# Optimization experiments

Measured on AMD Instinct MI355X. Metric: run time of the kernel, lower is better.

## Reference

```python
import jax, jax.numpy as jnp
import numpy as np

N_NODES = 100000
N_EDGES = 3200000


def gcn_conv(x, src, dst, W, b, n):
    # x: [N, Fin] -> linear transform then symmetric-normalized scatter-add (PyG GCNConv)
    xw = x @ W  # [N, Fout]
    loop = jnp.arange(n, dtype=src.dtype)
    s = jnp.concatenate([src, loop])  # add self-loops
    d = jnp.concatenate([dst, loop])
    deg = jax.ops.segment_sum(jnp.ones_like(s, dtype=xw.dtype), d, num_segments=n)
    dinv = jnp.where(deg > 0, jax.lax.rsqrt(deg), 0.0)
    norm = dinv[s] * dinv[d]  # [E+N]
    out = jax.ops.segment_sum(xw[s] * norm[:, None], d, num_segments=n)
    return out + b


def setup_inputs() -> dict:
    key = jax.random.key(0)
    ks = jax.random.split(key, 11)
    x = jax.random.normal(ks[0], (N_NODES, 2), dtype=jnp.float32)
    edge_index = jax.random.randint(ks[1], (2, N_EDGES), 0, N_NODES, dtype=jnp.int64)
    W1 = jax.random.normal(ks[2], (2, 32), dtype=jnp.float32) * 0.5
    b1 = jax.random.normal(ks[3], (32,), dtype=jnp.float32) * 0.1
    W2 = jax.random.normal(ks[4], (32, 32), dtype=jnp.float32) * 0.18
    b2 = jax.random.normal(ks[5], (32,), dtype=jnp.float32) * 0.1
    Wf1 = jax.random.normal(ks[6], (32, 32), dtype=jnp.float32) * 0.18
    bf1 = jax.random.normal(ks[7], (32,), dtype=jnp.float32) * 0.1
    Wf2 = jax.random.normal(ks[8], (32, 1), dtype=jnp.float32) * 0.18
    bf2 = jax.random.normal(ks[9], (1,), dtype=jnp.float32) * 0.1
    return {"x": x, "edge_index": edge_index, "W1": W1, "b1": b1, "W2": W2,
            "b2": b2, "Wf1": Wf1, "bf1": bf1, "Wf2": Wf2, "bf2": bf2}


def reference(x, edge_index, W1, b1, W2, b2, Wf1, bf1, Wf2, bf2):
    n = x.shape[0]
    src, dst = edge_index[0], edge_index[1]
    h = jax.nn.relu(gcn_conv(x, src, dst, W1, b1, n))
    h = jax.nn.relu(gcn_conv(h, src, dst, W2, b2, n))
    h = jax.nn.relu(h @ Wf1 + bf1)
    return h @ Wf2 + bf2  # [N, 1]
```

## Files before the change

### kernel.cpp

```cpp
#include <hip/hip_runtime.h>

#define NGRP 512
#define CAP  7424
#define PTHREADS 1024
#define NE   16
#define EPB  (PTHREADS * NE)
#define SRC_BITS 17
#define SRC_MASK 0x1FFFF

static __device__ __forceinline__ unsigned f2bf(float f) {
    unsigned u = __float_as_uint(f);
    return (u + 0x7FFFu + ((u >> 16) & 1u)) >> 16;
}
static __device__ __forceinline__ float bf2f_lo(unsigned u) { return __uint_as_float(u << 16); }
static __device__ __forceinline__ float bf2f_hi(unsigned u) { return __uint_as_float(u & 0xFFFF0000u); }


__global__ __launch_bounds__(PTHREADS) void k_partition(const int* __restrict__ ei, int* gcursor,
                                                        unsigned* __restrict__ pairs,
                                                        int E, int n, int GN) {
    __shared__ int cnt[NGRP];
    __shared__ int cur[NGRP];
    int tid = threadIdx.x;
    if (tid < NGRP) cnt[tid] = 0;
    __syncthreads();
    int base = blockIdx.x * EPB;
    int sreg[NE], dreg[NE];
#pragma unroll
    for (int k = 0; k < NE; ++k) {
        int e = base + tid + k * PTHREADS;
        int d = -1, s = 0;
        if (e < E) {
            s = ei[e];
            d = ei[E + e];
            if ((unsigned)s < (unsigned)n && (unsigned)d < (unsigned)n)
                atomicAdd(&cnt[d / GN], 1);
            else d = -1;
        }
        sreg[k] = s; dreg[k] = d;
    }
    __syncthreads();
    if (tid < NGRP) {
        int c = cnt[tid];
        int rel = c ? atomicAdd(&gcursor[tid], c) : 0;
        cur[tid] = tid * CAP + rel;
    }
    __syncthreads();
#pragma unroll
    for (int k = 0; k < NE; ++k) {
        int d = dreg[k];
        if (d >= 0) {
            int g = d / GN;
            int w = atomicAdd(&cur[g], 1);
            if (w < (g + 1) * CAP)
                pairs[w] = ((unsigned)(d - g * GN) << SRC_BITS) | (unsigned)sreg[k];
        }
    }
}

__global__ __launch_bounds__(512) void k_build(const int* __restrict__ gcursor,
                                               const unsigned* __restrict__ pairs,
                                               const float2* __restrict__ x2,
                                               int* __restrict__ rowStart, int* __restrict__ rowEnd,
                                               int* __restrict__ srclist, float* __restrict__ dinv,
                                               float2* __restrict__ z, int n, int GN) {
    __shared__ unsigned pl[CAP];
    __shared__ int cnt[512];
    __shared__ int cur[512];
    int g = blockIdx.x;
    int t = threadIdx.x;
    int gbeg = g * CAP;
    int m = gcursor[g];
    const int MCAP = CAP - 600;
    if (m > MCAP) m = MCAP;
    cnt[t] = 0;
    if (g == 0 && t == 0) z[n] = make_float2(0.f, 0.f);
    __syncthreads();
    for (int k = t; k < m; k += 512) {
        unsigned v = pairs[gbeg + k];
        pl[k] = v;
        atomicAdd(&cnt[(v >> SRC_BITS) & 511], 1);
    }
    __syncthreads();
    int c = cnt[t];
    int rnd = (c + 3) & ~3;
    __syncthreads();
    cnt[t] = rnd;
    __syncthreads();
    for (int off = 1; off < 512; off <<= 1) {
        int add = (t >= off) ? cnt[t - off] : 0;
        __syncthreads();
        cnt[t] += add;
        __syncthreads();
    }
    int excl = cnt[t] - rnd;
    int node = g * GN + t;
    int st = gbeg + excl;
    if (t < GN && node < n) {
        rowStart[node] = st;
        rowEnd[node] = st + rnd;
        float di = rsqrtf(1.0f + (float)c);
        dinv[node] = di;
        float2 xv = x2[node];
        z[node] = make_float2(xv.x * di, xv.y * di);
        for (int j = c; j < rnd; ++j) srclist[st + j] = n;
    }
    cur[t] = excl;
    __syncthreads();
    for (int k = t; k < m; k += 512) {
        unsigned v = pl[k];
        int dl = (v >> SRC_BITS) & 511;
        int pos = atomicAdd(&cur[dl], 1);
        srclist[gbeg + pos] = (int)(v & SRC_MASK);
    }
}


__global__ __launch_bounds__(256) void k_mid1f(const int* __restrict__ rowStart,
                                               const int* __restrict__ rowEnd,
                                               const int* __restrict__ srclist,
                                               const float2* __restrict__ z,
                                               const float* __restrict__ dinv,
                                               const float* __restrict__ W1,
                                               const float* __restrict__ b1,
                                               const float* __restrict__ W2,
                                               unsigned short* __restrict__ y0,
                                               unsigned short* __restrict__ y1, int n) {
    __shared__ float sW[1024];
    __shared__ float sh[8][33];
    int tid = threadIdx.x;
    for (int k = tid; k < 1024; k += 256) sW[k] = W2[k];
    int ln = tid >> 5, f = tid & 31;
    int i = blockIdx.x * 8 + ln;
    float ax = 0.f, ay = 0.f;
    if (i < n) {
        int e = rowStart[i] + f, end = rowEnd[i];
        for (; e < end; e += 32) {
            float2 v = z[srclist[e]];
            ax += v.x; ay += v.y;
        }
    }
#pragma unroll
    for (int m = 1; m < 32; m <<= 1) {
        ax += __shfl_xor(ax, m, 64);
        ay += __shfl_xor(ay, m, 64);
    }
    float h = 0.f, di = 0.f;
    if (i < n) {
        di = dinv[i];
        float2 zz = z[i];
        ax += zz.x; ay += zz.y;
        h = di * (ax * W1[f] + ay * W1[32 + f]) + b1[f];
        h = h > 0.f ? h : 0.f;
    }
    sh[ln][f] = h;
    __syncthreads();
    if (i < n) {
        float acc = 0.f;
#pragma unroll
        for (int k = 0; k < 32; ++k) acc += sh[ln][k] * sW[k * 32 + f];
        unsigned short* ypl = (f < 16) ? y0 : y1;
        ypl[(size_t)i * 16 + (f & 15)] = (unsigned short)f2bf(acc * di);
    } else if (i == n) {
        unsigned short* ypl = (f < 16) ? y0 : y1;
        ypl[(size_t)n * 16 + (f & 15)] = 0;
    }
}

#define ACC8(v)                                        \
    a0 += bf2f_lo((v).x); a1 += bf2f_hi((v).x);        \
    a2 += bf2f_lo((v).y); a3 += bf2f_hi((v).y);        \
    a4 += bf2f_lo((v).z); a5 += bf2f_hi((v).z);        \
    a6 += bf2f_lo((v).w); a7 += bf2f_hi((v).w);

__global__ __launch_bounds__(256) void k_gather_planes(const int* __restrict__ rowStart,
                                                       const int* __restrict__ rowEnd,
                                                       const int* __restrict__ srclist,
                                                       const uint4* __restrict__ yp0,
                                                       const uint4* __restrict__ yp1,
                                                       const float* __restrict__ dinv,
                                                       const float* __restrict__ b2,
                                                       unsigned short* __restrict__ h2_0,
                                                       unsigned short* __restrict__ h2_1,
                                                       int n, int nb) {
    int blk = blockIdx.x;
    int p = (blk >> 2) & 1;
    int b = (blk >> 3) * 4 + (blk & 3);
    if (b >= nb) return;
    const uint4* yh = p ? yp1 : yp0;
    unsigned short* hp = p ? h2_1 : h2_0;
    int w = b * 64 + (threadIdx.x >> 2);
    if (w >= n) return;
    int slot = (threadIdx.x >> 1) & 1;
    int q = threadIdx.x & 1;
    int beg = rowStart[w];
    int nq = (rowEnd[w] - beg) >> 2;
    const int4* sl4 = (const int4*)(srclist + beg);
    float a0 = 0.f, a1 = 0.f, a2 = 0.f, a3 = 0.f, a4 = 0.f, a5 = 0.f, a6 = 0.f, a7 = 0.f;
    for (int j = slot; j < nq; j += 2) {
        int4 s4 = sl4[j];
        uint4 v0 = yh[(size_t)s4.x * 2 + q];
        uint4 v1 = yh[(size_t)s4.y * 2 + q];
        uint4 v2 = yh[(size_t)s4.z * 2 + q];
        uint4 v3 = yh[(size_t)s4.w * 2 + q];
        ACC8(v0); ACC8(v1); ACC8(v2); ACC8(v3);
    }
    if (slot == 0) {
        uint4 v = yh[(size_t)w * 2 + q];
        ACC8(v);
    }
    a0 += __shfl_xor(a0, 2, 64);
    a1 += __shfl_xor(a1, 2, 64);
    a2 += __shfl_xor(a2, 2, 64);
    a3 += __shfl_xor(a3, 2, 64);
    a4 += __shfl_xor(a4, 2, 64);
    a5 += __shfl_xor(a5, 2, 64);
    a6 += __shfl_xor(a6, 2, 64);
    a7 += __shfl_xor(a7, 2, 64);
    if (slot == 0) {
        float di = dinv[w];
        const float* bb = b2 + p * 16 + q * 8;
        float t0 = di * a0 + bb[0]; t0 = t0 > 0.f ? t0 : 0.f;
        float t1 = di * a1 + bb[1]; t1 = t1 > 0.f ? t1 : 0.f;
        float t2 = di * a2 + bb[2]; t2 = t2 > 0.f ? t2 : 0.f;
        float t3 = di * a3 + bb[3]; t3 = t3 > 0.f ? t3 : 0.f;
        float t4 = di * a4 + bb[4]; t4 = t4 > 0.f ? t4 : 0.f;
        float t5 = di * a5 + bb[5]; t5 = t5 > 0.f ? t5 : 0.f;
        float t6 = di * a6 + bb[6]; t6 = t6 > 0.f ? t6 : 0.f;
        float t7 = di * a7 + bb[7]; t7 = t7 > 0.f ? t7 : 0.f;
        uint4 pk;
        pk.x = f2bf(t0) | (f2bf(t1) << 16);
        pk.y = f2bf(t2) | (f2bf(t3) << 16);
        pk.z = f2bf(t4) | (f2bf(t5) << 16);
        pk.w = f2bf(t6) | (f2bf(t7) << 16);
        *(uint4*)(hp + (size_t)w * 16 + q * 8) = pk;
    }
}

__global__ void k_final(const unsigned short* __restrict__ h2_0,
                        const unsigned short* __restrict__ h2_1,
                        const float* __restrict__ Wf1, const float* __restrict__ bf1,
                        const float* __restrict__ Wf2, const float* __restrict__ bf2,
                        float* __restrict__ out, int n) {
    __shared__ float sW[1024];
    __shared__ float sh[8][33];
    int tid = threadIdx.x;
    for (int k = tid; k < 1024; k += 256) sW[k] = Wf1[k];
    int ln = tid >> 5, f = tid & 31;
    int i = blockIdx.x * 8 + ln;
    float h = 0.f;
    if (i < n) {
        const unsigned short* hp = (f < 16) ? h2_0 : h2_1;
        unsigned short u = hp[(size_t)i * 16 + (f & 15)];
        h = __uint_as_float((unsigned)u << 16);
    }
    sh[ln][f] = h;
    __syncthreads();
    float p = 0.f;
    if (i < n) {
        float a = bf1[f];
#pragma unroll
        for (int k = 0; k < 32; ++k) a += sh[ln][k] * sW[k * 32 + f];
        a = a > 0.f ? a : 0.f;
        p = a * Wf2[f];
    }
#pragma unroll
    for (int m = 16; m >= 1; m >>= 1) p += __shfl_xor(p, m, 64);
    if (f == 0 && i < n) out[i] = p + bf2[0];
}


extern "C" void kernel_launch(void* const* d_in, const int* in_sizes, int n_in,
                              void* d_out, int out_size, void* d_ws, size_t ws_size,
                              hipStream_t stream) {
    const float* x   = (const float*)d_in[0];
    const int*   ei  = (const int*)d_in[1];
    const float* W1  = (const float*)d_in[2];
    const float* b1  = (const float*)d_in[3];
    const float* W2  = (const float*)d_in[4];
    const float* b2  = (const float*)d_in[5];
    const float* Wf1 = (const float*)d_in[6];
    const float* bf1 = (const float*)d_in[7];
    const float* Wf2 = (const float*)d_in[8];
    const float* bf2 = (const float*)d_in[9];
    float* out = (float*)d_out;

    int n = in_sizes[0] / 2;
    int E = in_sizes[1] / 2;
    int GN = (n + NGRP - 1) / NGRP;

    char* wp = (char*)d_ws;
    auto alloc = [&](size_t bytes) {
        char* ptr = wp;
        wp += (bytes + 15) & ~(size_t)15;
        return ptr;
    };
    int*      srclist = (int*)     alloc(sizeof(int) * (size_t)NGRP * CAP);
    unsigned* pairs   = (unsigned*)alloc(sizeof(unsigned) * (size_t)NGRP * CAP);
    int*      rowStart= (int*)     alloc(sizeof(int) * (size_t)n);
    int*      rowEnd  = (int*)     alloc(sizeof(int) * (size_t)n);
    float*    dinv    = (float*)   alloc(sizeof(float) * (size_t)n);
    float2*   z       = (float2*)  alloc(sizeof(float2) * (size_t)(n + 1));
    int*      gcursor = (int*)     alloc(sizeof(int) * NGRP);
    unsigned short* y0  = (unsigned short*)alloc(2 * (size_t)(n + 1) * 16);
    unsigned short* y1  = (unsigned short*)alloc(2 * (size_t)(n + 1) * 16);
    unsigned short* h2_0= (unsigned short*)alloc(2 * (size_t)n * 16);
    unsigned short* h2_1= (unsigned short*)alloc(2 * (size_t)n * 16);

    int nblk = (E + EPB - 1) / EPB;
    int nb = (n + 63) / 64;
    int nsg = (nb + 3) / 4;

    (void)hipMemsetAsync(gcursor, 0, NGRP * sizeof(int), stream);
    k_partition<<<nblk, PTHREADS, 0, stream>>>(ei, gcursor, pairs, E, n, GN);
    k_build<<<NGRP, 512, 0, stream>>>(gcursor, pairs, (const float2*)x, rowStart, rowEnd,
                                      srclist, dinv, z, n, GN);

    k_mid1f<<<(n + 8) / 8, 256, 0, stream>>>(rowStart, rowEnd, srclist, z, dinv,
                                             W1, b1, W2, y0, y1, n);

    k_gather_planes<<<nsg * 8, 256, 0, stream>>>(rowStart, rowEnd, srclist,
                                                 (const uint4*)y0, (const uint4*)y1,
                                                 dinv, b2, h2_0, h2_1, n, nb);

    k_final<<<(n + 7) / 8, 256, 0, stream>>>(h2_0, h2_1, Wf1, bf1, Wf2, bf2, out, n);
}
```

Before: 160.0 us.

## Replicate partition counters and split layer-1 gather into thread-per-node kernel

The partition kernel now keeps four replicas of the per-group shared counters and cursors, indexed by thread lane, to reduce LDS atomic contention. The first-layer aggregation is split out of the fused kernel into its own kernel that assigns one thread per node, reads sources four at a time with int4 loads, and writes a float2 aggregate. A separate kernel then applies W1, ReLU and W2. This avoids leaving most of a 32-lane group idle on rows averaging about 32 edges, at the cost of an extra launch and a round trip of the aggregate through global memory. The int4 loop assumes each row's padded length is a multiple of four and that row starts are 16-byte aligned.

```diff
diff --git a/kernel.cpp b/kernel.cpp
--- a/kernel.cpp
+++ b/kernel.cpp
@@ -5,6 +5,7 @@
 #define PTHREADS 1024
 #define NE   16
 #define EPB  (PTHREADS * NE)
+#define NREP 4
 #define SRC_BITS 17
 #define SRC_MASK 0x1FFFF
 
@@ -19,10 +20,11 @@
 __global__ __launch_bounds__(PTHREADS) void k_partition(const int* __restrict__ ei, int* gcursor,
                                                         unsigned* __restrict__ pairs,
                                                         int E, int n, int GN) {
-    __shared__ int cnt[NGRP];
-    __shared__ int cur[NGRP];
+    __shared__ int cnt[NGRP][NREP];
+    __shared__ int cur[NGRP][NREP];
     int tid = threadIdx.x;
-    if (tid < NGRP) cnt[tid] = 0;
+    int r = tid & (NREP - 1);
+    for (int k = tid; k < NGRP * NREP; k += PTHREADS) ((int*)cnt)[k] = 0;
     __syncthreads();
     int base = blockIdx.x * EPB;
     int sreg[NE], dreg[NE];
@@ -34,16 +36,21 @@
             s = ei[e];
             d = ei[E + e];
             if ((unsigned)s < (unsigned)n && (unsigned)d < (unsigned)n)
-                atomicAdd(&cnt[d / GN], 1);
+                atomicAdd(&cnt[d / GN][r], 1);
             else d = -1;
         }
         sreg[k] = s; dreg[k] = d;
     }
     __syncthreads();
     if (tid < NGRP) {
-        int c = cnt[tid];
-        int rel = c ? atomicAdd(&gcursor[tid], c) : 0;
-        cur[tid] = tid * CAP + rel;
+        int c0 = cnt[tid][0], c1 = cnt[tid][1], c2 = cnt[tid][2], c3 = cnt[tid][3];
+        int tot = c0 + c1 + c2 + c3;
+        int rel = tot ? atomicAdd(&gcursor[tid], tot) : 0;
+        int b0 = tid * CAP + rel;
+        cur[tid][0] = b0;
+        cur[tid][1] = b0 + c0;
+        cur[tid][2] = b0 + c0 + c1;
+        cur[tid][3] = b0 + c0 + c1 + c2;
     }
     __syncthreads();
 #pragma unroll
@@ -51,7 +58,7 @@
         int d = dreg[k];
         if (d >= 0) {
             int g = d / GN;
-            int w = atomicAdd(&cur[g], 1);
+            int w = atomicAdd(&cur[g][r], 1);
             if (w < (g + 1) * CAP)
                 pairs[w] = ((unsigned)(d - g * GN) << SRC_BITS) | (unsigned)sreg[k];
         }
@@ -116,41 +123,42 @@
 }
 
 
-__global__ __launch_bounds__(256) void k_mid1f(const int* __restrict__ rowStart,
-                                               const int* __restrict__ rowEnd,
-                                               const int* __restrict__ srclist,
-                                               const float2* __restrict__ z,
-                                               const float* __restrict__ dinv,
-                                               const float* __restrict__ W1,
-                                               const float* __restrict__ b1,
-                                               const float* __restrict__ W2,
-                                               unsigned short* __restrict__ y0,
-                                               unsigned short* __restrict__ y1, int n) {
+__global__ __launch_bounds__(256) void k_gather2f(const int* __restrict__ rowStart,
+                                                  const int* __restrict__ rowEnd,
+                                                  const int* __restrict__ srclist,
+                                                  const float2* __restrict__ z,
+                                                  float2* __restrict__ agg, int n) {
+    int w = blockIdx.x * 256 + threadIdx.x;
+    if (w >= n) return;
+    int beg = rowStart[w];
+    int nq = (rowEnd[w] - beg) >> 2;
+    const int4* sl4 = (const int4*)(srclist + beg);
+    float ax = 0.f, ay = 0.f;
+    for (int j = 0; j < nq; ++j) {
+        int4 s4 = sl4[j];
+        float2 v0 = z[s4.x], v1 = z[s4.y], v2 = z[s4.z], v3 = z[s4.w];
+        ax += v0.x + v1.x + v2.x + v3.x;
+        ay += v0.y + v1.y + v2.y + v3.y;
+    }
+    float2 zz = z[w];
+    agg[w] = make_float2(ax + zz.x, ay + zz.y);
+}
+
+__global__ void k_mid1(const float2* __restrict__ agg, const float* __restrict__ dinv,
+                       const float* __restrict__ W1, const float* __restrict__ b1,
+                       const float* __restrict__ W2, unsigned short* __restrict__ y0,
+                       unsigned short* __restrict__ y1, int n) {
     __shared__ float sW[1024];
     __shared__ float sh[8][33];
     int tid = threadIdx.x;
     for (int k = tid; k < 1024; k += 256) sW[k] = W2[k];
     int ln = tid >> 5, f = tid & 31;
     int i = blockIdx.x * 8 + ln;
-    float ax = 0.f, ay = 0.f;
-    if (i < n) {
-        int e = rowStart[i] + f, end = rowEnd[i];
-        for (; e < end; e += 32) {
-            float2 v = z[srclist[e]];
-            ax += v.x; ay += v.y;
-        }
-    }
-#pragma unroll
-    for (int m = 1; m < 32; m <<= 1) {
-        ax += __shfl_xor(ax, m, 64);
-        ay += __shfl_xor(ay, m, 64);
-    }
     float h = 0.f, di = 0.f;
     if (i < n) {
         di = dinv[i];
-        float2 zz = z[i];
-        ax += zz.x; ay += zz.y;
-        h = di * (ax * W1[f] + ay * W1[32 + f]) + b1[f];
+        float2 a = agg[i];
+        h = di * (a.x * W1[f] + a.y * W1[32 + f]) + b1[f];
         h = h > 0.f ? h : 0.f;
     }
     sh[ln][f] = h;
@@ -301,6 +309,7 @@
     int*      rowEnd  = (int*)     alloc(sizeof(int) * (size_t)n);
     float*    dinv    = (float*)   alloc(sizeof(float) * (size_t)n);
     float2*   z       = (float2*)  alloc(sizeof(float2) * (size_t)(n + 1));
+    float2*   agg     = (float2*)  alloc(sizeof(float2) * (size_t)n);
     int*      gcursor = (int*)     alloc(sizeof(int) * NGRP);
     unsigned short* y0  = (unsigned short*)alloc(2 * (size_t)(n + 1) * 16);
     unsigned short* y1  = (unsigned short*)alloc(2 * (size_t)(n + 1) * 16);
@@ -316,8 +325,8 @@
     k_build<<<NGRP, 512, 0, stream>>>(gcursor, pairs, (const float2*)x, rowStart, rowEnd,
                                       srclist, dinv, z, n, GN);
 
-    k_mid1f<<<(n + 8) / 8, 256, 0, stream>>>(rowStart, rowEnd, srclist, z, dinv,
-                                             W1, b1, W2, y0, y1, n);
+    k_gather2f<<<(n + 255) / 256, 256, 0, stream>>>(rowStart, rowEnd, srclist, z, agg, n);
+    k_mid1<<<(n + 8) / 8, 256, 0, stream>>>(agg, dinv, W1, b1, W2, y0, y1, n);
 
     k_gather_planes<<<nsg * 8, 256, 0, stream>>>(rowStart, rowEnd, srclist,
                                                  (const uint4*)y0, (const uint4*)y1,
```

Result: slower. 168.8 us (+5.5%).
